# Kernel tuning notes

Measured on AMD Instinct MI355X. Metric: run time of the kernel, lower is better.

## Reference

```python
import jax, jax.numpy as jnp
import numpy as np

N_NODES = 170000
N_EDGES = 1200000
IN_DIM = 64
OUT_DIM = 40


def setup_inputs() -> dict:
    key = jax.random.key(0)
    k1, k2, k3, k4 = jax.random.split(key, 4)
    feats = jax.random.normal(k1, (N_NODES, IN_DIM), dtype=jnp.float32)
    # Linear layer params (Kaiming-ish scale)
    W = jax.random.normal(k2, (OUT_DIM, IN_DIM), dtype=jnp.float32) * (1.0 / np.sqrt(IN_DIM))
    b = jnp.zeros((OUT_DIM,), dtype=jnp.float32)
    src = jax.random.randint(k3, (N_EDGES,), 0, N_NODES, dtype=jnp.int64)
    dst = jax.random.randint(k4, (N_EDGES,), 0, N_NODES, dtype=jnp.int64)
    return {"feats": feats, "W": W, "b": b, "src": src, "dst": dst}


def reference(feats, W, b, src, dst):
    # DGL SGConv, k=1: symmetric normalization by in-degree^-1/2 on both sides.
    n = feats.shape[0]
    deg = jax.ops.segment_sum(jnp.ones_like(dst, dtype=feats.dtype), dst, num_segments=n)
    norm = jax.lax.rsqrt(jnp.maximum(deg, 1.0))  # clamp(min=1)
    h = feats * norm[:, None]                    # [N, D] pre-scale
    msgs = jnp.take(h, src, axis=0)              # [E, D] gather
    agg = jax.ops.segment_sum(msgs, dst, num_segments=n)  # [N, D] scatter-sum
    h = agg * norm[:, None]                      # post-scale
    out = jnp.einsum('nd,cd->nc', h, W) + b      # Linear(IN_DIM -> OUT_DIM)
    return out
```

## Files before the change

### kernel.cpp

```cpp
#include <hip/hip_runtime.h>
#include <hip/hip_bf16.h>

#define N_NODES 170000
#define N_EDGES 1200000
#define IN_DIM 64
#define OUT_DIM 40
#define PAD 32
#define ZW 20
#define MTILES (N_NODES / 16)
#define TFB ((MTILES + 3) / 4)
#define SEGS 8
#define SEG_SZ (N_NODES / SEGS)
#define SLICES 512
#define SLICE_E ((N_EDGES + SLICES - 1) / SLICES)
#define FILLB (SLICES * SEGS)
#define FUSED_BLOCKS (FILLB + TFB)
#define GWAVES (N_NODES / 2)
#define PRER 3

typedef __attribute__((ext_vector_type(8))) short short8;
typedef __attribute__((ext_vector_type(4))) float f32x4;

__device__ __forceinline__ float bf2f(unsigned int u) {
    union { unsigned int i; float f; } v;
    v.i = u << 16;
    return v.f;
}

__device__ __forceinline__ unsigned short f2bf_bits(float x) {
    __hip_bfloat16 h = __float2bfloat16(x);
    union { __hip_bfloat16 h; unsigned short u; } c; c.h = h;
    return c.u;
}

__global__ void __launch_bounds__(256) k_fused(
    const void* __restrict__ src, const void* __restrict__ dst,
    int* __restrict__ cnt, int* __restrict__ slots,
    const void* __restrict__ feats, const unsigned short* __restrict__ Wraw,
    const unsigned short* __restrict__ braw, float* __restrict__ bfv,
    unsigned short* __restrict__ Zp16) {
    int bid = blockIdx.x;
    int do_fill, id;
    if (bid < 2 * TFB) { do_fill = bid & 1; id = bid >> 1; }
    else               { do_fill = 1;       id = bid - TFB; }

    __shared__ int sh_flag;
    if (threadIdx.x == 0) sh_flag = 0;
    __syncthreads();

    if (do_fill) {
        if (((const unsigned int*)dst)[2 * threadIdx.x + 1] != 0u) atomicOr(&sh_flag, 1);
        __syncthreads();
        int is_i32 = sh_flag;

        int seg   = id & 7;
        int slice = id >> 3;
        int lo = seg * SEG_SZ, hi = lo + SEG_SZ;
        int e0 = slice * SLICE_E;
        int e1 = e0 + SLICE_E; if (e1 > N_EDGES) e1 = N_EDGES;
        if (is_i32) {
            const int* dp = (const int*)dst;
            const int* sp = (const int*)src;
            int nE = e1 - e0;
            int nV = nE >> 2;
            const int4* dv = (const int4*)(dp + e0);
            const int4* sv = (const int4*)(sp + e0);
            for (int q = (int)threadIdx.x; q < nV; q += 256) {
                int4 d4 = dv[q];
                int4 s4 = sv[q];
                if (d4.x >= lo && d4.x < hi) {
                    int pos = atomicAdd(&cnt[d4.x], 1);
                    if (pos < PAD) slots[(size_t)d4.x * PAD + pos] = s4.x;
                }
                if (d4.y >= lo && d4.y < hi) {
                    int pos = atomicAdd(&cnt[d4.y], 1);
                    if (pos < PAD) slots[(size_t)d4.y * PAD + pos] = s4.y;
                }
                if (d4.z >= lo && d4.z < hi) {
                    int pos = atomicAdd(&cnt[d4.z], 1);
                    if (pos < PAD) slots[(size_t)d4.z * PAD + pos] = s4.z;
                }
                if (d4.w >= lo && d4.w < hi) {
                    int pos = atomicAdd(&cnt[d4.w], 1);
                    if (pos < PAD) slots[(size_t)d4.w * PAD + pos] = s4.w;
                }
            }
            int rem = nE & 3;
            if ((int)threadIdx.x < rem) {
                int e = e0 + (nV << 2) + (int)threadIdx.x;
                int d = dp[e];
                if (d >= lo && d < hi) {
                    int pos = atomicAdd(&cnt[d], 1);
                    if (pos < PAD) slots[(size_t)d * PAD + pos] = sp[e];
                }
            }
        } else {
            const long long* dp = (const long long*)dst;
            const long long* sp = (const long long*)src;
            for (int e = e0 + (int)threadIdx.x; e < e1; e += 256) {
                int d = (int)dp[e];
                if (d >= lo && d < hi) {
                    int s = (int)sp[e];
                    int pos = atomicAdd(&cnt[d], 1);
                    if (pos < PAD) slots[(size_t)d * PAD + pos] = s;
                }
            }
        }
    } else {
        for (int i = threadIdx.x; i < OUT_DIM * IN_DIM; i += 256) {
            float v = bf2f(Wraw[i]);
            if (!(fabsf(v) <= 100.0f)) atomicOr(&sh_flag, 1);
        }
        __syncthreads();
        int is_f32 = sh_flag;
        if (bid == 0 && threadIdx.x < OUT_DIM)
            bfv[threadIdx.x] = is_f32 ? ((const float*)braw)[threadIdx.x]
                                      : bf2f(braw[threadIdx.x]);

        int wave = id * 4 + (int)(threadIdx.x >> 6);
        int lane = threadIdx.x & 63;
        if (wave >= MTILES) return;
        int m = lane & 15;
        int quad = lane >> 4;
        int node0 = wave * 16;

        short8 a0, a1;
        if (is_f32) {
            const float* frow = (const float*)feats + (size_t)(node0 + m) * IN_DIM + quad * 8;
            float4 p0 = *(const float4*)(frow + 0);
            float4 p1 = *(const float4*)(frow + 4);
            float4 p2 = *(const float4*)(frow + 32);
            float4 p3 = *(const float4*)(frow + 36);
            a0[0] = (short)f2bf_bits(p0.x); a0[1] = (short)f2bf_bits(p0.y);
            a0[2] = (short)f2bf_bits(p0.z); a0[3] = (short)f2bf_bits(p0.w);
            a0[4] = (short)f2bf_bits(p1.x); a0[5] = (short)f2bf_bits(p1.y);
            a0[6] = (short)f2bf_bits(p1.z); a0[7] = (short)f2bf_bits(p1.w);
            a1[0] = (short)f2bf_bits(p2.x); a1[1] = (short)f2bf_bits(p2.y);
            a1[2] = (short)f2bf_bits(p2.z); a1[3] = (short)f2bf_bits(p2.w);
            a1[4] = (short)f2bf_bits(p3.x); a1[5] = (short)f2bf_bits(p3.y);
            a1[6] = (short)f2bf_bits(p3.z); a1[7] = (short)f2bf_bits(p3.w);
        } else {
            const unsigned short* frow = (const unsigned short*)feats + (size_t)(node0 + m) * IN_DIM + quad * 8;
            a0 = *(const short8*)(frow);
            a1 = *(const short8*)(frow + 32);
        }

        f32x4 c0 = {0.f, 0.f, 0.f, 0.f}, c1 = c0, c2 = c0;
#pragma unroll
        for (int t = 0; t < 3; t++) {
            int n = t * 16 + m;
            bool ok = (n < OUT_DIM);
            short8 b0, b1;
#pragma unroll
            for (int j = 0; j < 8; j++) { b0[j] = 0; b1[j] = 0; }
            if (ok) {
                if (is_f32) {
                    const float* wrow = (const float*)Wraw + (size_t)n * IN_DIM + quad * 8;
                    float4 w0 = *(const float4*)(wrow + 0);
                    float4 w1 = *(const float4*)(wrow + 4);
                    float4 w2 = *(const float4*)(wrow + 32);
                    float4 w3 = *(const float4*)(wrow + 36);
                    b0[0] = (short)f2bf_bits(w0.x); b0[1] = (short)f2bf_bits(w0.y);
                    b0[2] = (short)f2bf_bits(w0.z); b0[3] = (short)f2bf_bits(w0.w);
                    b0[4] = (short)f2bf_bits(w1.x); b0[5] = (short)f2bf_bits(w1.y);
                    b0[6] = (short)f2bf_bits(w1.z); b0[7] = (short)f2bf_bits(w1.w);
                    b1[0] = (short)f2bf_bits(w2.x); b1[1] = (short)f2bf_bits(w2.y);
                    b1[2] = (short)f2bf_bits(w2.z); b1[3] = (short)f2bf_bits(w2.w);
                    b1[4] = (short)f2bf_bits(w3.x); b1[5] = (short)f2bf_bits(w3.y);
                    b1[6] = (short)f2bf_bits(w3.z); b1[7] = (short)f2bf_bits(w3.w);
                } else {
                    const unsigned short* wrow = Wraw + (size_t)n * IN_DIM + quad * 8;
                    b0 = *(const short8*)(wrow);
                    b1 = *(const short8*)(wrow + 32);
                }
            }
            if (t == 0) {
                c0 = __builtin_amdgcn_mfma_f32_16x16x32_bf16(a0, b0, c0, 0, 0, 0);
                c0 = __builtin_amdgcn_mfma_f32_16x16x32_bf16(a1, b1, c0, 0, 0, 0);
            } else if (t == 1) {
                c1 = __builtin_amdgcn_mfma_f32_16x16x32_bf16(a0, b0, c1, 0, 0, 0);
                c1 = __builtin_amdgcn_mfma_f32_16x16x32_bf16(a1, b1, c1, 0, 0, 0);
            } else {
                c2 = __builtin_amdgcn_mfma_f32_16x16x32_bf16(a0, b0, c2, 0, 0, 0);
                c2 = __builtin_amdgcn_mfma_f32_16x16x32_bf16(a1, b1, c2, 0, 0, 0);
            }
        }

        int r0 = quad * 4;
#pragma unroll
        for (int r = 0; r < 4; r++) {
            size_t base = (size_t)(node0 + r0 + r) * OUT_DIM;
            Zp16[base + m]      = f2bf_bits(c0[r]);
            Zp16[base + 16 + m] = f2bf_bits(c1[r]);
            if (m < 8)
                Zp16[base + 32 + m] = f2bf_bits(c2[r]);
        }
    }
}

__global__ void __launch_bounds__(256) k_gather(
    const int* __restrict__ cnt, const int* __restrict__ slots,
    const unsigned int* __restrict__ Zp, const float* __restrict__ bfv,
    float* __restrict__ out) {
    int wid = (blockIdx.x * blockDim.x + threadIdx.x) >> 6;
    int lane = threadIdx.x & 63;
    if (wid >= GWAVES) return;
    int nA = wid * 2, nB = nA + 1;

    int deg_my = cnt[nA + (lane >> 5)];
    int deg_ot = __shfl(deg_my, lane ^ 32);
    int degA = (lane < 32) ? deg_my : deg_ot;
    int degB = (lane < 32) ? deg_ot : deg_my;
    int dcA = degA > PAD ? PAD : degA;
    int dcB = degB > PAD ? PAD : degB;
    int dcm = dcA > dcB ? dcA : dcB;

    int myslot = slots[(size_t)(nA + (lane >> 5)) * PAD + (lane & 31)];

    int grp = lane / 5;
    int cidx = lane - grp * 5;
    bool lact = (grp < 12);
    int side = (grp >= 6) ? 1 : 0;
    int g6 = grp - side * 6;
    int dcS = side ? dcB : dcA;
    int sbase = side * 32;

    float a0 = 0.f, a1 = 0.f, a2 = 0.f, a3 = 0.f;
    float a4 = 0.f, a5 = 0.f, a6 = 0.f, a7 = 0.f;

    uint4 rr[PRER];
    int   cd[PRER];
    int   vv[PRER];
#pragma unroll
    for (int rd = 0; rd < PRER; rd++) {
        vv[rd] = 0;
        if (rd * 6 < dcm) {
            int e1 = rd * 6 + g6;
            bool v1 = lact && (e1 < dcS);
            int s1 = __shfl(myslot, sbase + (v1 ? e1 : 0));
            s1 = v1 ? s1 : 0;
            rr[rd] = *(const uint4*)(Zp + (size_t)s1 * ZW + 4 * cidx);
            cd[rd] = cnt[s1];
            vv[rd] = v1 ? 1 : 0;
        }
    }
#pragma unroll
    for (int rd = 0; rd < PRER; rd++) {
        if (rd * 6 < dcm && vv[rd]) {
            float nvs = rsqrtf(cd[rd] > 1 ? (float)cd[rd] : 1.0f);
            a0 = fmaf(bf2f(rr[rd].x & 0xFFFFu), nvs, a0);
            a1 = fmaf(bf2f(rr[rd].x >> 16),     nvs, a1);
            a2 = fmaf(bf2f(rr[rd].y & 0xFFFFu), nvs, a2);
            a3 = fmaf(bf2f(rr[rd].y >> 16),     nvs, a3);
            a4 = fmaf(bf2f(rr[rd].z & 0xFFFFu), nvs, a4);
            a5 = fmaf(bf2f(rr[rd].z >> 16),     nvs, a5);
            a6 = fmaf(bf2f(rr[rd].w & 0xFFFFu), nvs, a6);
            a7 = fmaf(bf2f(rr[rd].w >> 16),     nvs, a7);
        }
    }
    for (int rd = PRER; rd * 6 < dcm; rd++) {
        int e1 = rd * 6 + g6;
        bool v1 = lact && (e1 < dcS);
        int s1 = __shfl(myslot, sbase + (v1 ? e1 : 0));
        s1 = v1 ? s1 : 0;
        uint4 r = *(const uint4*)(Zp + (size_t)s1 * ZW + 4 * cidx);
        int cn = cnt[s1];
        if (v1) {
            float nvs = rsqrtf(cn > 1 ? (float)cn : 1.0f);
            a0 = fmaf(bf2f(r.x & 0xFFFFu), nvs, a0);
            a1 = fmaf(bf2f(r.x >> 16),     nvs, a1);
            a2 = fmaf(bf2f(r.y & 0xFFFFu), nvs, a2);
            a3 = fmaf(bf2f(r.y >> 16),     nvs, a3);
            a4 = fmaf(bf2f(r.z & 0xFFFFu), nvs, a4);
            a5 = fmaf(bf2f(r.z >> 16),     nvs, a5);
            a6 = fmaf(bf2f(r.w & 0xFFFFu), nvs, a6);
            a7 = fmaf(bf2f(r.w >> 16),     nvs, a7);
        }
    }

#define RED6(A) { float s_ = A + __shfl(A, (lane + 15) & 63); \
                  A = s_ + __shfl(s_, (lane + 5) & 63) + __shfl(s_, (lane + 10) & 63); }
    RED6(a0) RED6(a1) RED6(a2) RED6(a3) RED6(a4) RED6(a5) RED6(a6) RED6(a7)
#undef RED6

    bool wA = (lane < 5);
    bool wB = (lane >= 30 && lane < 35);
    if (wA || wB) {
        int nOut = wA ? nA : nB;
        int ci   = wA ? lane : (lane - 30);
        int dg   = wA ? degA : degB;
        float nv = rsqrtf(dg > 1 ? (float)dg : 1.0f);
        float* op = out + (size_t)nOut * OUT_DIM + 8 * ci;
        float4 o1, o2;
        o1.x = fmaf(a0, nv, bfv[8 * ci + 0]);
        o1.y = fmaf(a1, nv, bfv[8 * ci + 1]);
        o1.z = fmaf(a2, nv, bfv[8 * ci + 2]);
        o1.w = fmaf(a3, nv, bfv[8 * ci + 3]);
        o2.x = fmaf(a4, nv, bfv[8 * ci + 4]);
        o2.y = fmaf(a5, nv, bfv[8 * ci + 5]);
        o2.z = fmaf(a6, nv, bfv[8 * ci + 6]);
        o2.w = fmaf(a7, nv, bfv[8 * ci + 7]);
        *reinterpret_cast<float4*>(op)     = o1;
        *reinterpret_cast<float4*>(op + 4) = o2;
    }
}

extern "C" void kernel_launch(void* const* d_in, const int* in_sizes, int n_in,
                              void* d_out, int out_size, void* d_ws, size_t ws_size,
                              hipStream_t stream) {
    const void* feats = d_in[0];
    const void* W     = d_in[1];
    const void* b     = d_in[2];
    const void* src   = d_in[3];
    const void* dst   = d_in[4];

    char* ws = (char*)d_ws;
    float*          bfv   = (float*)(ws + 256);
    int*            cnt   = (int*)(ws + 16384);
    int*            slots = (int*)(ws + 696448);
    unsigned short* Zp16  = (unsigned short*)(ws + 22456448);
    unsigned int*   Zp    = (unsigned int*)(ws + 22456448);

    (void)hipMemsetAsync(cnt, 0, 680000, stream);
    k_fused<<<FUSED_BLOCKS, 256, 0, stream>>>(src, dst, cnt, slots, feats,
                                              (const unsigned short*)W,
                                              (const unsigned short*)b, bfv, Zp16);
    k_gather<<<(GWAVES * 64 + 255) / 256, 256, 0, stream>>>(cnt, slots, Zp, bfv, (float*)d_out);
}
```

Measured before the change: 198.4 us.

## Replace memset with init kernel that precomputes dtype flags and bf16 weights

A small init kernel replaces the memset. It zeroes the degree counters, detects the weight and index dtypes once, and writes a bf16 copy of W and the float bias into workspace. The fused kernel then reads these flags instead of running a per-block detection pass with extra barriers, and loads W directly as bf16. The gather kernel issues its slot load first and drops the degree guard on the prefetch rounds, which adds some wasted loads for low-degree nodes in exchange for fewer branches.

```diff
diff --git a/kernel.cpp b/kernel.cpp
--- a/kernel.cpp
+++ b/kernel.cpp
@@ -33,26 +33,45 @@
     return c.u;
 }
 
+__global__ void __launch_bounds__(256) k_init(
+    const unsigned short* __restrict__ Wraw, const unsigned short* __restrict__ braw,
+    const unsigned int* __restrict__ dstraw, int* __restrict__ flags,
+    unsigned short* __restrict__ Wb, float* __restrict__ bfv, int* __restrict__ cnt) {
+    int tid = blockIdx.x * 256 + threadIdx.x;
+    int gsz = (int)gridDim.x * 256;
+    int4* c4 = (int4*)cnt;
+    for (int i = tid; i < 42500; i += gsz) c4[i] = make_int4(0, 0, 0, 0);
+    if (blockIdx.x != 0) return;
+
+    __shared__ int s_f32, s_i32;
+    if (threadIdx.x == 0) { s_f32 = 0; s_i32 = 0; }
+    __syncthreads();
+    for (int i = threadIdx.x; i < OUT_DIM * IN_DIM; i += 256) {
+        float v = bf2f(Wraw[i]);
+        if (!(fabsf(v) <= 100.0f)) atomicOr(&s_f32, 1);
+    }
+    if (dstraw[2 * threadIdx.x + 1] != 0u) atomicOr(&s_i32, 1);
+    __syncthreads();
+    int is_f32 = s_f32;
+    if (threadIdx.x == 0) { flags[0] = s_f32; flags[1] = s_i32; }
+    for (int i = threadIdx.x; i < OUT_DIM * IN_DIM; i += 256)
+        Wb[i] = is_f32 ? f2bf_bits(((const float*)Wraw)[i]) : Wraw[i];
+    for (int i = threadIdx.x; i < OUT_DIM; i += 256)
+        bfv[i] = is_f32 ? ((const float*)braw)[i] : bf2f(braw[i]);
+}
+
 __global__ void __launch_bounds__(256) k_fused(
     const void* __restrict__ src, const void* __restrict__ dst,
     int* __restrict__ cnt, int* __restrict__ slots,
-    const void* __restrict__ feats, const unsigned short* __restrict__ Wraw,
-    const unsigned short* __restrict__ braw, float* __restrict__ bfv,
-    unsigned short* __restrict__ Zp16) {
+    const void* __restrict__ feats, const unsigned short* __restrict__ Wb,
+    unsigned short* __restrict__ Zp16, const int* __restrict__ flags) {
     int bid = blockIdx.x;
     int do_fill, id;
     if (bid < 2 * TFB) { do_fill = bid & 1; id = bid >> 1; }
     else               { do_fill = 1;       id = bid - TFB; }
 
-    __shared__ int sh_flag;
-    if (threadIdx.x == 0) sh_flag = 0;
-    __syncthreads();
-
     if (do_fill) {
-        if (((const unsigned int*)dst)[2 * threadIdx.x + 1] != 0u) atomicOr(&sh_flag, 1);
-        __syncthreads();
-        int is_i32 = sh_flag;
-
+        int is_i32 = flags[1];
         int seg   = id & 7;
         int slice = id >> 3;
         int lo = seg * SEG_SZ, hi = lo + SEG_SZ;
@@ -107,16 +126,7 @@
             }
         }
     } else {
-        for (int i = threadIdx.x; i < OUT_DIM * IN_DIM; i += 256) {
-            float v = bf2f(Wraw[i]);
-            if (!(fabsf(v) <= 100.0f)) atomicOr(&sh_flag, 1);
-        }
-        __syncthreads();
-        int is_f32 = sh_flag;
-        if (bid == 0 && threadIdx.x < OUT_DIM)
-            bfv[threadIdx.x] = is_f32 ? ((const float*)braw)[threadIdx.x]
-                                      : bf2f(braw[threadIdx.x]);
-
+        int is_f32 = flags[0];
         int wave = id * 4 + (int)(threadIdx.x >> 6);
         int lane = threadIdx.x & 63;
         if (wave >= MTILES) return;
@@ -154,25 +164,9 @@
 #pragma unroll
             for (int j = 0; j < 8; j++) { b0[j] = 0; b1[j] = 0; }
             if (ok) {
-                if (is_f32) {
-                    const float* wrow = (const float*)Wraw + (size_t)n * IN_DIM + quad * 8;
-                    float4 w0 = *(const float4*)(wrow + 0);
-                    float4 w1 = *(const float4*)(wrow + 4);
-                    float4 w2 = *(const float4*)(wrow + 32);
-                    float4 w3 = *(const float4*)(wrow + 36);
-                    b0[0] = (short)f2bf_bits(w0.x); b0[1] = (short)f2bf_bits(w0.y);
-                    b0[2] = (short)f2bf_bits(w0.z); b0[3] = (short)f2bf_bits(w0.w);
-                    b0[4] = (short)f2bf_bits(w1.x); b0[5] = (short)f2bf_bits(w1.y);
-                    b0[6] = (short)f2bf_bits(w1.z); b0[7] = (short)f2bf_bits(w1.w);
-                    b1[0] = (short)f2bf_bits(w2.x); b1[1] = (short)f2bf_bits(w2.y);
-                    b1[2] = (short)f2bf_bits(w2.z); b1[3] = (short)f2bf_bits(w2.w);
-                    b1[4] = (short)f2bf_bits(w3.x); b1[5] = (short)f2bf_bits(w3.y);
-                    b1[6] = (short)f2bf_bits(w3.z); b1[7] = (short)f2bf_bits(w3.w);
-                } else {
-                    const unsigned short* wrow = Wraw + (size_t)n * IN_DIM + quad * 8;
-                    b0 = *(const short8*)(wrow);
-                    b1 = *(const short8*)(wrow + 32);
-                }
+                const unsigned short* wrow = Wb + (size_t)n * IN_DIM + quad * 8;
+                b0 = *(const short8*)(wrow);
+                b1 = *(const short8*)(wrow + 32);
             }
             if (t == 0) {
                 c0 = __builtin_amdgcn_mfma_f32_16x16x32_bf16(a0, b0, c0, 0, 0, 0);
@@ -207,6 +201,8 @@
     if (wid >= GWAVES) return;
     int nA = wid * 2, nB = nA + 1;
 
+    int myslot = slots[(size_t)(nA + (lane >> 5)) * PAD + (lane & 31)];
+
     int deg_my = cnt[nA + (lane >> 5)];
     int deg_ot = __shfl(deg_my, lane ^ 32);
     int degA = (lane < 32) ? deg_my : deg_ot;
@@ -215,8 +211,6 @@
     int dcB = degB > PAD ? PAD : degB;
     int dcm = dcA > dcB ? dcA : dcB;
 
-    int myslot = slots[(size_t)(nA + (lane >> 5)) * PAD + (lane & 31)];
-
     int grp = lane / 5;
     int cidx = lane - grp * 5;
     bool lact = (grp < 12);
@@ -233,20 +227,17 @@
     int   vv[PRER];
 #pragma unroll
     for (int rd = 0; rd < PRER; rd++) {
-        vv[rd] = 0;
-        if (rd * 6 < dcm) {
-            int e1 = rd * 6 + g6;
-            bool v1 = lact && (e1 < dcS);
-            int s1 = __shfl(myslot, sbase + (v1 ? e1 : 0));
-            s1 = v1 ? s1 : 0;
-            rr[rd] = *(const uint4*)(Zp + (size_t)s1 * ZW + 4 * cidx);
-            cd[rd] = cnt[s1];
-            vv[rd] = v1 ? 1 : 0;
-        }
+        int e1 = rd * 6 + g6;
+        bool v1 = lact && (e1 < dcS);
+        int s1 = __shfl(myslot, sbase + (v1 ? e1 : 0));
+        s1 = v1 ? s1 : 0;
+        rr[rd] = *(const uint4*)(Zp + (size_t)s1 * ZW + 4 * cidx);
+        cd[rd] = cnt[s1];
+        vv[rd] = v1 ? 1 : 0;
     }
 #pragma unroll
     for (int rd = 0; rd < PRER; rd++) {
-        if (rd * 6 < dcm && vv[rd]) {
+        if (vv[rd]) {
             float nvs = rsqrtf(cd[rd] > 1 ? (float)cd[rd] : 1.0f);
             a0 = fmaf(bf2f(rr[rd].x & 0xFFFFu), nvs, a0);
             a1 = fmaf(bf2f(rr[rd].x >> 16),     nvs, a1);
@@ -315,15 +306,16 @@
     const void* dst   = d_in[4];
 
     char* ws = (char*)d_ws;
+    int*            flags = (int*)(ws + 0);
     float*          bfv   = (float*)(ws + 256);
+    unsigned short* Wb    = (unsigned short*)(ws + 1024);
     int*            cnt   = (int*)(ws + 16384);
     int*            slots = (int*)(ws + 696448);
     unsigned short* Zp16  = (unsigned short*)(ws + 22456448);
     unsigned int*   Zp    = (unsigned int*)(ws + 22456448);
 
-    (void)hipMemsetAsync(cnt, 0, 680000, stream);
-    k_fused<<<FUSED_BLOCKS, 256, 0, stream>>>(src, dst, cnt, slots, feats,
-                                              (const unsigned short*)W,
-                                              (const unsigned short*)b, bfv, Zp16);
+    k_init<<<256, 256, 0, stream>>>((const unsigned short*)W, (const unsigned short*)b,
+                                    (const unsigned int*)dst, flags, Wb, bfv, cnt);
+    k_fused<<<FUSED_BLOCKS, 256, 0, stream>>>(src, dst, cnt, slots, feats, Wb, Zp16, flags);
     k_gather<<<(GWAVES * 64 + 255) / 256, 256, 0, stream>>>(cnt, slots, Zp, bfv, (float*)d_out);
 }
```

New measurement: 190.6 us. -3.9%, faster.
